# Kernel optimization log

Hardware: AMD Instinct MI355X
Metric: run time of the kernel (lower is better)

## Reference

```python
import jax, jax.numpy as jnp
import numpy as np

B, N, M = 2, 2048, 2048
D_K, D_V, H = 256, 256, 8
D_KS = D_K // H  # 32, per-head key dim (ceil(256/8))
D_VS = D_V // H  # 32
MASK_BIG = 1e32


def setup_inputs() -> dict:
    key = jax.random.key(0)
    ks = jax.random.split(key, 10)
    s = 0.02
    queries = jax.random.normal(ks[0], (B, N, D_K), jnp.float32)
    keys_ = jax.random.normal(ks[1], (B, M, D_K), jnp.float32)
    values = jax.random.normal(ks[2], (B, M, D_V), jnp.float32)
    presence = (jax.random.uniform(ks[3], (B, M)) > 0.3).astype(jnp.float32)
    Wq = jax.random.normal(ks[4], (D_K, D_KS * H), jnp.float32) * s
    bq = jnp.zeros((D_KS * H,), jnp.float32)
    Wk = jax.random.normal(ks[5], (D_K, D_KS * H), jnp.float32) * s
    bk = jnp.zeros((D_KS * H,), jnp.float32)
    Wv = jax.random.normal(ks[6], (D_V, D_VS * H), jnp.float32) * s
    bv = jnp.zeros((D_VS * H,), jnp.float32)
    Wo = jax.random.normal(ks[7], (D_VS * H, D_V), jnp.float32) * s
    bo = jnp.zeros((D_V,), jnp.float32)
    return {"queries": queries, "keys": keys_, "values": values, "presence": presence,
            "Wq": Wq, "bq": bq, "Wk": Wk, "bk": bk, "Wv": Wv, "bv": bv, "Wo": Wo, "bo": bo}


def reference(queries, keys, values, presence, Wq, bq, Wk, bk, Wv, bv, Wo, bo):
    # Project and split into heads. torch's split(d_k_s,-1)+cat(...,0) puts the
    # head index as the outer batch dim; a [B,N,H,d] reshape is the same math.
    q = (queries @ Wq + bq).reshape(B, N, H, D_KS)
    k = (keys @ Wk + bk).reshape(B, M, H, D_KS)
    v = (values @ Wv + bv).reshape(B, M, H, D_VS)
    # Raw scores, additive presence mask, then scale by sqrt(per-head d_k)
    scores = jnp.einsum('bnhd,bmhd->bhnm', q, k)
    scores = scores - (1.0 - presence)[:, None, None, :] * MASK_BIG
    attn = jax.nn.softmax(scores / np.sqrt(D_KS).astype(np.float32), axis=-1)
    o = jnp.einsum('bhnm,bmhd->bnhd', attn, v).reshape(B, N, H * D_VS)
    return o @ Wo + bo
```

## Files before the change

### kernel.cpp

```cpp
#include <hip/hip_runtime.h>

#define B_ 2
#define N_ 2048
#define M_ 2048
#define D_ 256
#define H_ 8
#define DH_ 32
#define SPLITS 2
#define QSCALE (0.17677669529663689f * 1.4426950408889634f)

typedef __attribute__((ext_vector_type(8))) short short8;
typedef __attribute__((ext_vector_type(4))) float f32x4;
typedef unsigned short u16;
typedef unsigned int u32;

#if __has_builtin(__builtin_amdgcn_exp2f)
#define EXP2 __builtin_amdgcn_exp2f
#else
#define EXP2 exp2f
#endif

union u4s8 { uint4 u; short8 s; };

__device__ __forceinline__ u16 f2bf(float f) {
  u32 u = __float_as_uint(f);
  return (u16)((u + 0x7fffu + ((u >> 16) & 1u)) >> 16);
}
__device__ __forceinline__ u32 cvtpk_bf16(float lo, float hi) {
  u32 r;
  asm("v_cvt_pk_bf16_f32 %0, %1, %2" : "=v"(r) : "v"(lo), "v"(hi));
  return r;
}
__device__ __forceinline__ void gload_lds16(const u16* g, u16* l) {
  __builtin_amdgcn_global_load_lds((const __attribute__((address_space(1))) void*)g,
                                   (__attribute__((address_space(3))) void*)l, 16, 0, 0);
}
__device__ __forceinline__ void gload_lds16f(const float* g, float* l) {
  __builtin_amdgcn_global_load_lds((const __attribute__((address_space(1))) void*)g,
                                   (__attribute__((address_space(3))) void*)l, 16, 0, 0);
}

__global__ __launch_bounds__(256, 2) void qkvproj_kernel(
    const float* __restrict__ Xq, const float* __restrict__ Xk, const float* __restrict__ Xv,
    const float* __restrict__ Wq, const float* __restrict__ Wk, const float* __restrict__ Wv,
    const float* __restrict__ bq, const float* __restrict__ bk, const float* __restrict__ bv,
    u16* __restrict__ qb, u16* __restrict__ kb, u16* __restrict__ vtb) {
  __shared__ u16 wsT[64 * 256];
  __shared__ u16 xs[64 * 256];
  const int p = blockIdx.y;
  const int nb = blockIdx.x & 63, cb = blockIdx.x >> 6;
  const int n0B = nb * 64, c0B = cb * 64;
  const float* X = p == 0 ? Xq : (p == 1 ? Xk : Xv);
  const float* W = p == 0 ? Wq : (p == 1 ? Wk : Wv);
  const float* bias = p == 0 ? bq : (p == 1 ? bk : bv);
  const int t = threadIdx.x;

  {
    const int cL = (t & 15) * 4, kB = (t >> 4) * 16;
    const float* wp = W + (size_t)kB * D_ + c0B + cL;
#pragma unroll
    for (int u = 0; u < 4; ++u) {
      const int k0 = kB + 4 * u;
      const f32x4 w0 = *(const f32x4*)(wp + (size_t)(4 * u + 0) * D_);
      const f32x4 w1 = *(const f32x4*)(wp + (size_t)(4 * u + 1) * D_);
      const f32x4 w2 = *(const f32x4*)(wp + (size_t)(4 * u + 2) * D_);
      const f32x4 w3 = *(const f32x4*)(wp + (size_t)(4 * u + 3) * D_);
#pragma unroll
      for (int cc = 0; cc < 4; ++cc) {
        const int c = cL + cc;
        uint2 v;
        v.x = cvtpk_bf16(w0[cc], w1[cc]);
        v.y = cvtpk_bf16(w2[cc], w3[cc]);
        *(uint2*)(wsT + c * 256 + (((k0 >> 3) ^ (c & 7)) * 8) + (k0 & 7)) = v;
      }
    }
  }
  {
    const int nL = t >> 2, k64 = (t & 3) * 64;
    const float* xp = X + (size_t)(n0B + nL) * D_ + k64;
#pragma unroll
    for (int m = 0; m < 8; ++m) {
      const f32x4 a = *(const f32x4*)(xp + 8 * m);
      const f32x4 b2 = *(const f32x4*)(xp + 8 * m + 4);
      uint4 v;
      v.x = cvtpk_bf16(a[0], a[1]);
      v.y = cvtpk_bf16(a[2], a[3]);
      v.z = cvtpk_bf16(b2[0], b2[1]);
      v.w = cvtpk_bf16(b2[2], b2[3]);
      const int k0 = k64 + 8 * m;
      *(uint4*)(xs + nL * 256 + (((k0 >> 3) ^ (nL & 7)) * 8)) = v;
    }
  }
  __syncthreads();

  const int wv = t >> 6, lane = t & 63, lr = lane & 15, lg = lane >> 4;
  const f32x4 zz = {0.f, 0.f, 0.f, 0.f};
  f32x4 acc[4] = {zz, zz, zz, zz};
  const int arow = wv * 16 + lr;
#pragma unroll
  for (int ks = 0; ks < 8; ++ks) {
    const short8 a = *(const short8*)(wsT + arow * 256 + (((ks * 4 + lg) ^ (arow & 7)) * 8));
#pragma unroll
    for (int ng = 0; ng < 4; ++ng) {
      const int brow = ng * 16 + lr;
      const short8 b = *(const short8*)(xs + brow * 256 + (((ks * 4 + lg) ^ (brow & 7)) * 8));
      acc[ng] = __builtin_amdgcn_mfma_f32_16x16x32_bf16(a, b, acc[ng], 0, 0, 0);
    }
  }

  const int cg4 = c0B + wv * 16 + lg * 4;
  const f32x4 bias4 = *(const f32x4*)(bias + cg4);
  if (p < 2) {
    u16* ob = p == 0 ? qb : kb;
    const float sc = p == 0 ? QSCALE : 1.0f;
#pragma unroll
    for (int ng = 0; ng < 4; ++ng) {
      const int n = n0B + ng * 16 + lr;
      const int b = n >> 11, nn = n & (N_ - 1);
#pragma unroll
      for (int j = 0; j < 4; ++j) {
        const int c = cg4 + j;
        ob[((size_t)(b * H_ + (c >> 5)) * N_ + nn) * DH_ + (c & 31)] =
            f2bf((acc[ng][j] + bias4[j]) * sc);
      }
    }
  } else {
#pragma unroll
    for (int ng = 0; ng < 4; ++ng) {
      const int n = n0B + ng * 16 + lr;
      const int b = n >> 11, nn = n & (M_ - 1);
#pragma unroll
      for (int j = 0; j < 4; ++j) {
        const int c = cg4 + j;
        vtb[((size_t)(b * H_ + (c >> 5)) * DH_ + (c & 31)) * M_ + nn] =
            f2bf(acc[ng][j] + bias4[j]);
      }
    }
  }
}

__global__ __launch_bounds__(256, 4) void attn_kernel(
    const u16* __restrict__ qb, const u16* __restrict__ kb,
    const u16* __restrict__ vtb, const float* __restrict__ presence,
    float* __restrict__ opart, float* __restrict__ lpart) {
  __shared__ u16 kvlds[2][4096];
  __shared__ float prlds[1024];
  const int t = threadIdx.x;
  const int wv = t >> 6, lane = t & 63;
  const int lr = lane & 15, lg = lane >> 4;
  const int s = blockIdx.x >> 9;
  const int bh = (blockIdx.x >> 5) & 15;
  const int qblk = blockIdx.x & 31;
  const int b = bh >> 3, h = bh & 7;
  const int n0 = qblk * 64 + wv * 16;
  const int m0 = s * (M_ / SPLITS);
  const int NI = (M_ / SPLITS) / 64;

  const int gsk = (t & 3) ^ ((t >> 3) & 3);
  const u16* kst = kb + ((size_t)bh * M_ + m0 + (t >> 2)) * DH_ + gsk * 8;
  const int gsv = (t & 7) ^ ((t >> 3) & 7);
  const u16* vst = vtb + ((size_t)bh * DH_ + (t >> 3)) * M_ + m0 + gsv * 8;
  u16* const ldswK = &kvlds[0][0] + wv * 512;
  u16* const ldswV = &kvlds[0][0] + 2048 + wv * 512;

  const int ko0 = lr * 32 + (lg ^ ((lr >> 1) & 3)) * 8;
  const int sw = lr & 7;
  const int vb = (((lg >> 1) ^ sw) * 8) + (lg & 1) * 4;

  const short8 qf = *(const short8*)(qb + ((size_t)bh * N_ + n0 + lr) * DH_ + lg * 8);

  const f32x4 zz = {0.f, 0.f, 0.f, 0.f};
  f32x4 o0 = zz, o1 = zz, racc = zz;

  gload_lds16(kst, ldswK);
  gload_lds16(vst, ldswV);
  gload_lds16f(presence + (size_t)b * M_ + m0 + wv * 256 + lane * 4, prlds + wv * 256);
  __syncthreads();

#pragma unroll 2
  for (int i = 0; i < NI; ++i) {
    const int mm = i * 64;
    const u16* kl = &kvlds[i & 1][0];
    const u16* vl = &kvlds[i & 1][2048];
    if (i + 1 < NI) {
      const int bo = ((i + 1) & 1) * 4096;
      gload_lds16(kst + (size_t)(i + 1) * (64 * DH_), ldswK + bo);
      gload_lds16(vst + (size_t)(i + 1) * 64, ldswV + bo);
    }

    f32x4 s4[4];
    __builtin_amdgcn_s_setprio(1);
#pragma unroll
    for (int tt = 0; tt < 4; ++tt) {
      const short8 kf = *(const short8*)(kl + tt * 512 + ko0);
      s4[tt] = __builtin_amdgcn_mfma_f32_16x16x32_bf16(kf, qf, zz, 0, 0, 0);
    }
    __builtin_amdgcn_s_setprio(0);

#pragma unroll
    for (int tt = 0; tt < 4; ++tt) {
      const f32x4 pr = *(const f32x4*)(prlds + mm + tt * 16 + lg * 4);
#pragma unroll
      for (int j = 0; j < 4; ++j) s4[tt][j] = EXP2(s4[tt][j]);
      s4[tt] *= pr;
      racc += s4[tt];
    }
    u4s8 pm0, pm1;
    pm0.u.x = cvtpk_bf16(s4[0][0], s4[0][1]);
    pm0.u.y = cvtpk_bf16(s4[0][2], s4[0][3]);
    pm0.u.z = cvtpk_bf16(s4[1][0], s4[1][1]);
    pm0.u.w = cvtpk_bf16(s4[1][2], s4[1][3]);
    pm1.u.x = cvtpk_bf16(s4[2][0], s4[2][1]);
    pm1.u.y = cvtpk_bf16(s4[2][2], s4[2][3]);
    pm1.u.z = cvtpk_bf16(s4[3][0], s4[3][1]);
    pm1.u.w = cvtpk_bf16(s4[3][2], s4[3][3]);

    const u16* vr0 = vl + lr * 64;
    const u16* vr1 = vl + (16 + lr) * 64;
    u4s8 vm0, vm1, vm2, vm3;
    {
      const uint2 e0 = *(const uint2*)(vr0 + (vb ^ 0));
      const uint2 e1 = *(const uint2*)(vr0 + (vb ^ 16));
      const uint2 e2 = *(const uint2*)(vr0 + (vb ^ 32));
      const uint2 e3 = *(const uint2*)(vr0 + (vb ^ 48));
      vm0.u = make_uint4(e0.x, e0.y, e1.x, e1.y);
      vm1.u = make_uint4(e2.x, e2.y, e3.x, e3.y);
      const uint2 f0 = *(const uint2*)(vr1 + (vb ^ 0));
      const uint2 f1 = *(const uint2*)(vr1 + (vb ^ 16));
      const uint2 f2 = *(const uint2*)(vr1 + (vb ^ 32));
      const uint2 f3 = *(const uint2*)(vr1 + (vb ^ 48));
      vm2.u = make_uint4(f0.x, f0.y, f1.x, f1.y);
      vm3.u = make_uint4(f2.x, f2.y, f3.x, f3.y);
    }
    __builtin_amdgcn_s_setprio(1);
    o0 = __builtin_amdgcn_mfma_f32_16x16x32_bf16(pm0.s, vm0.s, o0, 0, 0, 0);
    o0 = __builtin_amdgcn_mfma_f32_16x16x32_bf16(pm1.s, vm1.s, o0, 0, 0, 0);
    o1 = __builtin_amdgcn_mfma_f32_16x16x32_bf16(pm0.s, vm2.s, o1, 0, 0, 0);
    o1 = __builtin_amdgcn_mfma_f32_16x16x32_bf16(pm1.s, vm3.s, o1, 0, 0, 0);
    __builtin_amdgcn_s_setprio(0);
    __syncthreads();
  }

  float l = (racc[0] + racc[1]) + (racc[2] + racc[3]);
  l += __shfl_xor(l, 16);
  l += __shfl_xor(l, 32);
  if (lg == 0) lpart[((size_t)s * (B_ * N_) + b * N_ + n0 + lr) * H_ + h] = l;

  float* ob = opart + ((size_t)s * (B_ * N_) + (size_t)b * N_ + n0) * D_ + h * DH_;
#pragma unroll
  for (int j = 0; j < 4; ++j) {
    const int q = lg * 4 + j;
    ob[(size_t)q * D_ + lr] = o0[j];
    ob[(size_t)q * D_ + 16 + lr] = o1[j];
  }
}

__global__ __launch_bounds__(256, 2) void projo_kernel(
    const float* __restrict__ opart, const float* __restrict__ lpart,
    const float* __restrict__ Wo, const float* __restrict__ bo,
    float* __restrict__ out) {
  __shared__ u16 wsT[64 * 256];
  __shared__ u16 xs[64 * 256];
  const int nb = blockIdx.x & 63, cb = blockIdx.x >> 6;
  const int n0B = nb * 64, c0B = cb * 64;
  const int t = threadIdx.x;

  {
    const int cL = (t & 15) * 4, kB = (t >> 4) * 16;
    const float* wp = Wo + (size_t)kB * D_ + c0B + cL;
#pragma unroll
    for (int u = 0; u < 4; ++u) {
      const int k0 = kB + 4 * u;
      const f32x4 w0 = *(const f32x4*)(wp + (size_t)(4 * u + 0) * D_);
      const f32x4 w1 = *(const f32x4*)(wp + (size_t)(4 * u + 1) * D_);
      const f32x4 w2 = *(const f32x4*)(wp + (size_t)(4 * u + 2) * D_);
      const f32x4 w3 = *(const f32x4*)(wp + (size_t)(4 * u + 3) * D_);
#pragma unroll
      for (int cc = 0; cc < 4; ++cc) {
        const int c = cL + cc;
        uint2 v;
        v.x = cvtpk_bf16(w0[cc], w1[cc]);
        v.y = cvtpk_bf16(w2[cc], w3[cc]);
        *(uint2*)(wsT + c * 256 + (((k0 >> 3) ^ (c & 7)) * 8) + (k0 & 7)) = v;
      }
    }
  }
  {
    const int nL = t >> 2, k64 = (t & 3) * 64;
    const int gn = n0B + nL;
    const int h0 = k64 >> 5;
    float l0s = 0.f, l1s = 0.f;
#pragma unroll
    for (int sp = 0; sp < SPLITS; ++sp) {
      l0s += lpart[((size_t)sp * (B_ * N_) + gn) * H_ + h0];
      l1s += lpart[((size_t)sp * (B_ * N_) + gn) * H_ + h0 + 1];
    }
    const float il0 = 1.f / l0s, il1 = 1.f / l1s;
    const float* obase = opart + (size_t)gn * D_ + k64;
#pragma unroll
    for (int m = 0; m < 8; ++m) {
      f32x4 a = {0.f, 0.f, 0.f, 0.f};
      f32x4 b2 = {0.f, 0.f, 0.f, 0.f};
#pragma unroll
      for (int sp = 0; sp < SPLITS; ++sp) {
        const float* op = obase + (size_t)sp * (B_ * N_) * D_;
        a += *(const f32x4*)(op + 8 * m);
        b2 += *(const f32x4*)(op + 8 * m + 4);
      }
      const float il = (m < 4) ? il0 : il1;
      a *= il;
      b2 *= il;
      uint4 v;
      v.x = cvtpk_bf16(a[0], a[1]);
      v.y = cvtpk_bf16(a[2], a[3]);
      v.z = cvtpk_bf16(b2[0], b2[1]);
      v.w = cvtpk_bf16(b2[2], b2[3]);
      const int k0 = k64 + 8 * m;
      *(uint4*)(xs + nL * 256 + (((k0 >> 3) ^ (nL & 7)) * 8)) = v;
    }
  }
  __syncthreads();

  const int wv = t >> 6, lane = t & 63, lr = lane & 15, lg = lane >> 4;
  const f32x4 zz = {0.f, 0.f, 0.f, 0.f};
  f32x4 acc[4] = {zz, zz, zz, zz};
  const int arow = wv * 16 + lr;
#pragma unroll
  for (int ks = 0; ks < 8; ++ks) {
    const short8 a = *(const short8*)(xs + arow * 256 + (((ks * 4 + lg) ^ (arow & 7)) * 8));
#pragma unroll
    for (int ng = 0; ng < 4; ++ng) {
      const int brow = ng * 16 + lr;
      const short8 bfr = *(const short8*)(wsT + brow * 256 + (((ks * 4 + lg) ^ (brow & 7)) * 8));
      acc[ng] = __builtin_amdgcn_mfma_f32_16x16x32_bf16(a, bfr, acc[ng], 0, 0, 0);
    }
  }
#pragma unroll
  for (int ng = 0; ng < 4; ++ng) {
    const int c = c0B + ng * 16 + lr;
    const float bb = bo[c];
#pragma unroll
    for (int j = 0; j < 4; ++j)
      out[(size_t)(n0B + wv * 16 + lg * 4 + j) * D_ + c] = acc[ng][j] + bb;
  }
}

extern "C" void kernel_launch(void* const* d_in, const int* in_sizes, int n_in,
                              void* d_out, int out_size, void* d_ws, size_t ws_size,
                              hipStream_t stream) {
  (void)in_sizes; (void)n_in; (void)out_size; (void)ws_size;
  const float* queries  = (const float*)d_in[0];
  const float* keys     = (const float*)d_in[1];
  const float* values   = (const float*)d_in[2];
  const float* presence = (const float*)d_in[3];
  const float* Wq = (const float*)d_in[4];
  const float* bq = (const float*)d_in[5];
  const float* Wk = (const float*)d_in[6];
  const float* bk = (const float*)d_in[7];
  const float* Wv = (const float*)d_in[8];
  const float* bv = (const float*)d_in[9];
  const float* Wo = (const float*)d_in[10];
  const float* bo = (const float*)d_in[11];

  u16* qb  = (u16*)d_ws;
  u16* kb  = qb + (size_t)B_ * H_ * N_ * DH_;
  u16* vtb = kb + (size_t)B_ * H_ * M_ * DH_;
  float* opart = (float*)(vtb + (size_t)B_ * H_ * DH_ * M_);
  float* lpart = opart + (size_t)SPLITS * B_ * N_ * D_;

  qkvproj_kernel<<<dim3(256, 3), 256, 0, stream>>>(
      queries, keys, values, Wq, Wk, Wv, bq, bk, bv, qb, kb, vtb);
  attn_kernel<<<SPLITS * 16 * 32, 256, 0, stream>>>(qb, kb, vtb, presence, opart, lpart);
  projo_kernel<<<256, 256, 0, stream>>>(opart, lpart, Wo, bo, (float*)d_out);
}
```

Baseline: 44.46 us.

## Triple-buffer K/V LDS tiles with prefetch distance two and partial vmcnt waits

Expands the K/V shared-memory staging from two to three buffers and issues global-to-LDS loads two iterations ahead. The full __syncthreads at the end of each iteration becomes an explicit s_waitcnt vmcnt that only waits for the older stage, followed by a raw s_barrier. This is meant to hide more global-load latency behind the QK/PV MFMA work. In exchange it uses more LDS, which may affect occupancy, and it drops the loop unroll pragma. Correctness now relies on hand-counted outstanding load counts.

```diff
diff --git a/kernel.cpp b/kernel.cpp
--- a/kernel.cpp
+++ b/kernel.cpp
@@ -143,7 +143,7 @@
     const u16* __restrict__ qb, const u16* __restrict__ kb,
     const u16* __restrict__ vtb, const float* __restrict__ presence,
     float* __restrict__ opart, float* __restrict__ lpart) {
-  __shared__ u16 kvlds[2][4096];
+  __shared__ u16 kvlds[3][4096];
   __shared__ float prlds[1024];
   const int t = threadIdx.x;
   const int wv = t >> 6, lane = t & 63;
@@ -160,8 +160,6 @@
   const u16* kst = kb + ((size_t)bh * M_ + m0 + (t >> 2)) * DH_ + gsk * 8;
   const int gsv = (t & 7) ^ ((t >> 3) & 7);
   const u16* vst = vtb + ((size_t)bh * DH_ + (t >> 3)) * M_ + m0 + gsv * 8;
-  u16* const ldswK = &kvlds[0][0] + wv * 512;
-  u16* const ldswV = &kvlds[0][0] + 2048 + wv * 512;
 
   const int ko0 = lr * 32 + (lg ^ ((lr >> 1) & 3)) * 8;
   const int sw = lr & 7;
@@ -172,21 +170,26 @@
   const f32x4 zz = {0.f, 0.f, 0.f, 0.f};
   f32x4 o0 = zz, o1 = zz, racc = zz;
 
-  gload_lds16(kst, ldswK);
-  gload_lds16(vst, ldswV);
+#define STAGE(it, bb) do {                                              \
+    u16* base_ = &kvlds[bb][0];                                         \
+    gload_lds16(kst + (size_t)(it) * (64 * DH_), base_ + wv * 512);     \
+    gload_lds16(vst + (size_t)(it) * 64, base_ + 2048 + wv * 512);      \
+  } while (0)
+
   gload_lds16f(presence + (size_t)b * M_ + m0 + wv * 256 + lane * 4, prlds + wv * 256);
-  __syncthreads();
-
-#pragma unroll 2
+  STAGE(0, 0);
+  STAGE(1, 1);
+  asm volatile("s_waitcnt vmcnt(2)" ::: "memory");
+  __builtin_amdgcn_sched_barrier(0);
+  __builtin_amdgcn_s_barrier();
+  __builtin_amdgcn_sched_barrier(0);
+
   for (int i = 0; i < NI; ++i) {
     const int mm = i * 64;
-    const u16* kl = &kvlds[i & 1][0];
-    const u16* vl = &kvlds[i & 1][2048];
-    if (i + 1 < NI) {
-      const int bo = ((i + 1) & 1) * 4096;
-      gload_lds16(kst + (size_t)(i + 1) * (64 * DH_), ldswK + bo);
-      gload_lds16(vst + (size_t)(i + 1) * 64, ldswV + bo);
-    }
+    const u16* kl = &kvlds[i % 3][0];
+    const u16* vl = kl + 2048;
+    const bool more = (i + 2 < NI);
+    if (more) STAGE(i + 2, (i + 2) % 3);
 
     f32x4 s4[4];
     __builtin_amdgcn_s_setprio(1);
@@ -238,8 +241,17 @@
     o1 = __builtin_amdgcn_mfma_f32_16x16x32_bf16(pm0.s, vm2.s, o1, 0, 0, 0);
     o1 = __builtin_amdgcn_mfma_f32_16x16x32_bf16(pm1.s, vm3.s, o1, 0, 0, 0);
     __builtin_amdgcn_s_setprio(0);
-    __syncthreads();
-  }
+
+    if (more) {
+      asm volatile("s_waitcnt vmcnt(2)" ::: "memory");
+    } else {
+      asm volatile("s_waitcnt vmcnt(0)" ::: "memory");
+    }
+    __builtin_amdgcn_sched_barrier(0);
+    __builtin_amdgcn_s_barrier();
+    __builtin_amdgcn_sched_barrier(0);
+  }
+#undef STAGE
 
   float l = (racc[0] + racc[1]) + (racc[2] + racc[3]);
   l += __shfl_xor(l, 16);
```

Result: slower. 47.49 us (+6.8%).
